# Performance work log

Measured on AMD Instinct MI355X. Metric: run time of the kernel, lower is better.

Reference implementation:

```python
import jax, jax.numpy as jnp
import numpy as np

E = 8        # num_experts
TOP_K = 2
DIM = 1024
DFF = DIM // 4
T = 32768    # batch*seq tokens


def setup_inputs() -> dict:
    key = jax.random.key(0)
    ks = jax.random.split(key, 5)
    x = jax.random.normal(ks[0], (T, DIM), dtype=jnp.float32)
    router_w = jax.random.normal(ks[1], (E, DIM), dtype=jnp.float32) * 0.02
    w1 = jax.random.normal(ks[2], (E, DIM, DFF), dtype=jnp.float32) * 0.02
    w2 = jax.random.normal(ks[3], (E, DFF, DIM), dtype=jnp.float32) * 0.02
    w3 = jax.random.normal(ks[4], (E, DIM, DFF), dtype=jnp.float32) * 0.02
    return {"x": x, "router_w": router_w, "w1": w1, "w2": w2, "w3": w3}


def reference(x, router_w, w1, w2, w3):
    # ---- Router ----
    logits = x @ router_w.T                          # [T, E]
    scores = jax.nn.softmax(logits.astype(jnp.float32), axis=1)
    # expert_bias is zero at init and noise_scale=0 -> topk on raw scores
    _, sel = jax.lax.top_k(scores, TOP_K)            # [T, K] expert indices
    top_scores = jnp.take_along_axis(scores, sel, axis=-1)
    top_scores = top_scores / jnp.sum(top_scores, axis=-1, keepdims=True)

    flat_experts = sel.reshape(-1)                   # [T*K]
    sorted_idx = jnp.argsort(flat_experts)           # stable sort, expert-centric order
    scatter_idx = sorted_idx // TOP_K                # original token id per row
    num_tokens_per_expert = jnp.bincount(flat_experts, length=E).astype(jnp.int32)

    x_gathered = x[scatter_idx]                      # [T*K, DIM]
    scores_sorted = top_scores.reshape(-1)[sorted_idx]  # [T*K]

    # ---- GroupedExpert: grouped GEMM SwiGLU in bf16 ----
    xb = x_gathered.astype(jnp.bfloat16)
    x1 = jax.lax.ragged_dot(xb, w1.astype(jnp.bfloat16), num_tokens_per_expert)
    x3 = jax.lax.ragged_dot(xb, w3.astype(jnp.bfloat16), num_tokens_per_expert)
    h = jax.nn.silu(x1) * x3                         # [T*K, DFF] bf16
    expert_out = jax.lax.ragged_dot(h, w2.astype(jnp.bfloat16), num_tokens_per_expert)
    expert_out = expert_out.astype(x.dtype)          # [T*K, DIM]

    # ---- Combine: weighted scatter-add back to token positions ----
    out = jnp.zeros_like(x).at[scatter_idx].add(expert_out * scores_sorted[:, None])
    return out
```

## Files before the change

### kernel.cpp

```cpp
#include <hip/hip_runtime.h>
#include <cstdint>
#include <cstddef>
#include <math.h>

#define T_TOK 32768
#define DIM   1024
#define DFF   256
#define NE    8
#define NB    16
#define ROWS  (T_TOK * 2)
#define MAXROWS 66560
#define MAXTILES (MAXROWS / 64)

typedef unsigned short u16;
typedef __attribute__((ext_vector_type(8))) short v8s;
typedef __attribute__((ext_vector_type(4))) float v4f;

__device__ __forceinline__ u16 f2bf(float f) {
  union { float f; unsigned u; } v; v.f = f;
  return (u16)((v.u + 0x7FFFu + ((v.u >> 16) & 1u)) >> 16);
}
__device__ __forceinline__ float bf2f(u16 b) {
  union { unsigned u; float f; } v; v.u = ((unsigned)b) << 16; return v.f;
}

__device__ __forceinline__ void gload16(const u16* g, u16* l) {
  __builtin_amdgcn_global_load_lds(
      (const __attribute__((address_space(1))) void*)g,
      (__attribute__((address_space(3))) void*)l, 16, 0, 0);
}

#define WS_W13  ((size_t)0)
#define WS_W2T  ((size_t)8388608)
#define WS_H    ((size_t)12582912)
#define WS_Y    ((size_t)46661632)
#define WS_RTOK ((size_t)182976512)
#define WS_POS  ((size_t)183242752)
#define WS_CNT  ((size_t)183504896)
#define WS_CUR  ((size_t)183504960)
#define WS_OFF  ((size_t)183505024)
#define WS_SEL  ((size_t)183505152)
#define WS_WTS  ((size_t)183767296)
#define WS_XB   WS_Y

__global__ __launch_bounds__(256) void k_pack13(const float* __restrict__ w1,
                                                const float* __restrict__ w3,
                                                u16* __restrict__ W13p) {
  __shared__ float s1[32][33];
  __shared__ float s3[32][33];
  int e = blockIdx.z, k0 = blockIdx.x * 32, j0w = blockIdx.y;
  int tx = threadIdx.x, ty = threadIdx.y;
  size_t wbase = (size_t)e * DIM * DFF;
#pragma unroll
  for (int r = 0; r < 4; ++r) {
    int kl = ty + 8 * r;
    size_t src = wbase + (size_t)(k0 + kl) * DFF + j0w * 32 + tx;
    s1[kl][tx] = w1[src];
    s3[kl][tx] = w3[src];
  }
  __syncthreads();
  size_t obase = (size_t)e * 512 * 1024;
#pragma unroll
  for (int r = 0; r < 4; ++r) {
    int jl = ty + 8 * r;
    int n1 = 64 * j0w + jl;
    W13p[obase + (size_t)n1 * 1024 + k0 + tx]        = f2bf(s1[tx][jl]);
    W13p[obase + (size_t)(n1 + 32) * 1024 + k0 + tx] = f2bf(s3[tx][jl]);
  }
}

__global__ __launch_bounds__(256) void k_pack2(const float* __restrict__ w2,
                                               u16* __restrict__ W2t) {
  __shared__ float s[32][33];
  int e = blockIdx.z, k0 = blockIdx.x * 32, n0 = blockIdx.y * 32;
  int tx = threadIdx.x, ty = threadIdx.y;
#pragma unroll
  for (int r = 0; r < 4; ++r) {
    int kl = ty + 8 * r;
    s[kl][tx] = w2[(size_t)e * DFF * DIM + (size_t)(k0 + kl) * DIM + n0 + tx];
  }
  __syncthreads();
#pragma unroll
  for (int r = 0; r < 4; ++r) {
    int nl = ty + 8 * r;
    W2t[(size_t)e * DIM * DFF + (size_t)(n0 + nl) * DFF + k0 + tx] = f2bf(s[tx][nl]);
  }
}

__global__ __launch_bounds__(256) void k_router(const float* __restrict__ x,
                                                const float* __restrict__ rw,
                                                int* __restrict__ sel,
                                                float* __restrict__ wts,
                                                int* __restrict__ cnt,
                                                u16* __restrict__ xb) {
  __shared__ __align__(16) float s_rw[NE][1028];
  __shared__ __align__(16) float s_x[32][132];
  __shared__ float s_lg[256];
  __shared__ int s_cnt[NB];
  int tid = threadIdx.x;
  if (tid < NB) s_cnt[tid] = 0;
  {
    const float4* rw4 = (const float4*)rw;
#pragma unroll
    for (int r = 0; r < 8; ++r)
      *(float4*)(&s_rw[r][tid * 4]) = rw4[r * 256 + tid];
  }
  int tl = tid >> 3, e = tid & 7;
  float acc = 0.0f;
  const float4* x4 = (const float4*)x;
  for (int c = 0; c < 8; ++c) {
    __syncthreads();
#pragma unroll
    for (int j = 0; j < 4; ++j) {
      int slot = j * 256 + tid;
      int t = slot >> 5, kk = (slot & 31) * 4;
      *(float4*)(&s_x[t][kk]) = x4[((size_t)blockIdx.x * 32 + t) * 256 + c * 32 + (slot & 31)];
    }
    __syncthreads();
    const float* xp = &s_x[tl][0];
    const float* wp = &s_rw[e][c * 128];
#pragma unroll 16
    for (int k = 0; k < 128; ++k) acc = fmaf(xp[k], wp[k], acc);
    {
      int t2 = tid >> 3, k2 = (tid & 7) * 16;
      const float* sp = &s_x[t2][k2];
      u16 tb[16];
#pragma unroll
      for (int k = 0; k < 16; ++k) tb[k] = f2bf(sp[k]);
      u16* xo = xb + ((size_t)(blockIdx.x * 32 + t2)) * 1024 + c * 128 + k2;
      *(uint4*)(xo)     = *(const uint4*)(&tb[0]);
      *(uint4*)(xo + 8) = *(const uint4*)(&tb[8]);
    }
  }
  s_lg[tid] = acc;
  __syncthreads();
  if ((tid & 7) == 0) {
    int t = blockIdx.x * 32 + tl;
    const float* lg = s_lg + tid;
    int b0 = 0; float v0 = lg[0];
#pragma unroll
    for (int ee = 1; ee < NE; ++ee) if (lg[ee] > v0) { v0 = lg[ee]; b0 = ee; }
    int b1 = -1; float v1 = -1e30f;
#pragma unroll
    for (int ee = 0; ee < NE; ++ee) if (ee != b0 && lg[ee] > v1) { v1 = lg[ee]; b1 = ee; }
    float w0 = 1.0f / (1.0f + expf(v1 - v0));
    sel[2 * t] = b0; sel[2 * t + 1] = b1;
    wts[2 * t] = w0; wts[2 * t + 1] = 1.0f - w0;
    atomicAdd(&s_cnt[2 * b0], 1);
    atomicAdd(&s_cnt[2 * b1 + 1], 1);
  }
  __syncthreads();
  if (tid < NB && s_cnt[tid]) atomicAdd(&cnt[tid], s_cnt[tid]);
}

__global__ void k_scan(const int* __restrict__ cnt, int* __restrict__ offs) {
  if (threadIdx.x == 0 && blockIdx.x == 0) {
    int o = 0;
#pragma unroll
    for (int b = 0; b < NB; ++b) { offs[b] = o; o += (cnt[b] + 63) & ~63; }
    offs[NB] = o;
  }
}

__global__ __launch_bounds__(256) void k_scatter(const int* __restrict__ sel,
                                                 const int* __restrict__ offs,
                                                 int* __restrict__ cursor,
                                                 int* __restrict__ rtok,
                                                 int* __restrict__ pos) {
  __shared__ int s_cnt[NB], s_base[NB];
  int tid = threadIdx.x;
  if (tid < NB) s_cnt[tid] = 0;
  __syncthreads();
  int g = blockIdx.x * 256 + tid;
  int b = sel[g] * 2 + (g & 1);
  int lpos = atomicAdd(&s_cnt[b], 1);
  __syncthreads();
  if (tid < NB) s_base[tid] = s_cnt[tid] ? atomicAdd(&cursor[tid], s_cnt[tid]) : 0;
  __syncthreads();
  int row = offs[b] + s_base[b] + lpos;
  rtok[row] = g >> 1;
  pos[g] = row;
}

__global__ __launch_bounds__(512, 4) void k_gemm1(const u16* __restrict__ xb,
                                                  const u16* __restrict__ W13p,
                                                  const int* __restrict__ rtok,
                                                  const int* __restrict__ offs,
                                                  u16* __restrict__ h) {
  __shared__ __align__(16) u16 A_s[64][32];
  __shared__ __align__(16) u16 B_s[512][32];
  int bx = (int)((blockIdx.x & 7) * (MAXTILES / 8) + (blockIdx.x >> 3));
  int row0 = bx * 64;
  if (row0 >= offs[NB]) return;
  int b2 = 0;
  while (row0 >= offs[b2 + 1]) ++b2;
  int e = b2 >> 1;
  int tid = threadIdx.x;
  int wv = tid >> 6, lane = tid & 63;
  int lr = lane & 15, q = lane >> 4;
  int qa = q ^ ((lr >> 1) & 3);
  int srow = lane >> 2;
  int schk = (lane & 3) ^ ((lane >> 3) & 3);
  const u16* srcB = W13p + (size_t)e * 512 * 1024
                  + (size_t)(64 * wv + srow) * 1024 + schk * 8;
  int arow = (wv >= 4) ? (16 * (wv - 4) + srow) : srow;
  int tk = rtok[row0 + arow]; if (tk < 0) tk = 0;
  const u16* srcA = xb + (size_t)tk * 1024 + schk * 8;
  u16* ldsB = &B_s[64 * wv][0];
  u16* ldsA = &A_s[(wv & 3) * 16][0];
  v4f acc[4][4] = {};
  for (int k0 = 0; k0 < DIM; k0 += 32) {
#pragma unroll
    for (int i = 0; i < 4; ++i)
      gload16(srcB + (size_t)i * 16 * 1024 + k0, ldsB + i * 512);
    if (wv >= 4) gload16(srcA + k0, ldsA);
    __syncthreads();
    v8s a[4], b[4];
#pragma unroll
    for (int mt = 0; mt < 4; ++mt) a[mt] = *(const v8s*)(&A_s[16 * mt + lr][qa * 8]);
#pragma unroll
    for (int nt = 0; nt < 4; ++nt) b[nt] = *(const v8s*)(&B_s[64 * wv + 16 * nt + lr][qa * 8]);
#pragma unroll
    for (int mt = 0; mt < 4; ++mt)
#pragma unroll
      for (int nt = 0; nt < 4; ++nt)
        acc[mt][nt] = __builtin_amdgcn_mfma_f32_16x16x32_bf16(a[mt], b[nt], acc[mt][nt], 0, 0, 0);
    __syncthreads();
  }
#pragma unroll
  for (int mt = 0; mt < 4; ++mt)
#pragma unroll
    for (int nt = 0; nt < 2; ++nt)
#pragma unroll
      for (int r = 0; r < 4; ++r) {
        float x1 = bf2f(f2bf(acc[mt][nt][r]));
        float x3 = bf2f(f2bf(acc[mt][nt + 2][r]));
        float hv = x1 * x3 / (1.0f + __expf(-x1));
        int row = row0 + 16 * mt + q * 4 + r;
        int col = 32 * wv + 16 * nt + lr;
        h[(size_t)row * DFF + col] = f2bf(hv);
      }
}

__global__ __launch_bounds__(512, 4) void k_gemm2(const u16* __restrict__ h,
                                                  const u16* __restrict__ W2t,
                                                  const int* __restrict__ offs,
                                                  u16* __restrict__ y) {
  __shared__ __align__(16) u16 A_s[64][32];
  __shared__ __align__(16) u16 B_s[512][32];
  int bx = (int)((blockIdx.x & 7) * (MAXTILES / 8) + (blockIdx.x >> 3));
  int row0 = bx * 64;
  if (row0 >= offs[NB]) return;
  int b2 = 0;
  while (row0 >= offs[b2 + 1]) ++b2;
  int e = b2 >> 1;
  int nb = blockIdx.y;
  int tid = threadIdx.x;
  int wv = tid >> 6, lane = tid & 63;
  int lr = lane & 15, q = lane >> 4;
  int qa = q ^ ((lr >> 1) & 3);
  int srow = lane >> 2;
  int schk = (lane & 3) ^ ((lane >> 3) & 3);
  const u16* srcB = W2t + (size_t)e * DIM * DFF + (size_t)nb * 512 * DFF
                  + (size_t)(64 * wv + srow) * DFF + schk * 8;
  int arow = (wv >= 4) ? (16 * (wv - 4) + srow) : srow;
  const u16* srcA = h + (size_t)(row0 + arow) * DFF + schk * 8;
  u16* ldsB = &B_s[64 * wv][0];
  u16* ldsA = &A_s[(wv & 3) * 16][0];
  v4f acc[4][4] = {};
  for (int k0 = 0; k0 < DFF; k0 += 32) {
#pragma unroll
    for (int i = 0; i < 4; ++i)
      gload16(srcB + (size_t)i * 16 * DFF + k0, ldsB + i * 512);
    if (wv >= 4) gload16(srcA + k0, ldsA);
    __syncthreads();
    v8s a[4], b[4];
#pragma unroll
    for (int mt = 0; mt < 4; ++mt) a[mt] = *(const v8s*)(&A_s[16 * mt + lr][qa * 8]);
#pragma unroll
    for (int nt = 0; nt < 4; ++nt) b[nt] = *(const v8s*)(&B_s[64 * wv + 16 * nt + lr][qa * 8]);
#pragma unroll
    for (int mt = 0; mt < 4; ++mt)
#pragma unroll
      for (int nt = 0; nt < 4; ++nt)
        acc[mt][nt] = __builtin_amdgcn_mfma_f32_16x16x32_bf16(a[mt], b[nt], acc[mt][nt], 0, 0, 0);
    __syncthreads();
  }
  u16* Ts = &B_s[0][0];
#pragma unroll
  for (int mt = 0; mt < 4; ++mt) {
#pragma unroll
    for (int nt = 0; nt < 4; ++nt)
#pragma unroll
      for (int r = 0; r < 4; ++r)
        Ts[(q * 4 + r) * 520 + 64 * wv + 16 * nt + lr] = f2bf(acc[mt][nt][r]);
    __syncthreads();
#pragma unroll
    for (int i = 0; i < 2; ++i) {
      int j = tid + 512 * i;
      int rr = j >> 6, cc = j & 63;
      uint4 v = *(const uint4*)(Ts + rr * 520 + cc * 8);
      *(uint4*)(y + (size_t)(row0 + 16 * mt + rr) * 1024 + nb * 512 + cc * 8) = v;
    }
    __syncthreads();
  }
}

__global__ __launch_bounds__(256) void k_combine(const u16* __restrict__ y,
                                                 const int* __restrict__ pos,
                                                 const float* __restrict__ wts,
                                                 float* __restrict__ out) {
  int tid = threadIdx.x, wv = tid >> 6, lane = tid & 63;
  int t = blockIdx.x * 4 + wv;
  int r0 = pos[2 * t], r1 = pos[2 * t + 1];
  float w0 = wts[2 * t], w1 = wts[2 * t + 1];
  const uint4* y0 = (const uint4*)(y + (size_t)r0 * 1024);
  const uint4* y1 = (const uint4*)(y + (size_t)r1 * 1024);
  float* o = out + (size_t)t * 1024;
#pragma unroll
  for (int i = 0; i < 2; ++i) {
    int j = lane + 64 * i;
    uint4 a = y0[j], b = y1[j];
    const u16* pa = (const u16*)&a;
    const u16* pb = (const u16*)&b;
    float f[8];
#pragma unroll
    for (int k = 0; k < 8; ++k) f[k] = bf2f(pa[k]) * w0 + bf2f(pb[k]) * w1;
    *(float4*)(o + j * 8)     = *(float4*)&f[0];
    *(float4*)(o + j * 8 + 4) = *(float4*)&f[4];
  }
}

extern "C" void kernel_launch(void* const* d_in, const int* in_sizes, int n_in,
                              void* d_out, int out_size, void* d_ws, size_t ws_size,
                              hipStream_t stream) {
  (void)in_sizes; (void)n_in; (void)ws_size; (void)out_size;
  const float* x  = (const float*)d_in[0];
  const float* rw = (const float*)d_in[1];
  const float* w1 = (const float*)d_in[2];
  const float* w2 = (const float*)d_in[3];
  const float* w3 = (const float*)d_in[4];
  float* out = (float*)d_out;
  char* ws = (char*)d_ws;
  u16*   W13p = (u16*)(ws + WS_W13);
  u16*   W2t  = (u16*)(ws + WS_W2T);
  u16*   hbuf = (u16*)(ws + WS_H);
  u16*   ybuf = (u16*)(ws + WS_Y);
  u16*   xbuf = (u16*)(ws + WS_XB);
  int*   rtok = (int*)(ws + WS_RTOK);
  int*   pos  = (int*)(ws + WS_POS);
  int*   cnt  = (int*)(ws + WS_CNT);
  int*   cur  = (int*)(ws + WS_CUR);
  int*   offs = (int*)(ws + WS_OFF);
  int*   sel  = (int*)(ws + WS_SEL);
  float* wts  = (float*)(ws + WS_WTS);

  hipMemsetAsync(ws + WS_RTOK, 0xFF, (size_t)MAXROWS * 4, stream);
  hipMemsetAsync(ws + WS_CNT, 0, 128, stream);

  k_pack13<<<dim3(32, 8, 8), dim3(32, 8), 0, stream>>>(w1, w3, W13p);
  k_pack2 <<<dim3(8, 32, 8), dim3(32, 8), 0, stream>>>(w2, W2t);
  k_router<<<dim3(T_TOK / 32), dim3(256), 0, stream>>>(x, rw, sel, wts, cnt, xbuf);
  k_scan  <<<dim3(1), dim3(64), 0, stream>>>(cnt, offs);
  k_scatter<<<dim3(ROWS / 256), dim3(256), 0, stream>>>(sel, offs, cur, rtok, pos);
  k_gemm1 <<<dim3(MAXTILES), dim3(512), 0, stream>>>(xbuf, W13p, rtok, offs, hbuf);
  k_gemm2 <<<dim3(MAXTILES, 2), dim3(512), 0, stream>>>(hbuf, W2t, offs, ybuf);
  k_combine<<<dim3(T_TOK / 4), dim3(256), 0, stream>>>(ybuf, pos, wts, out);
}
```

Before: 494.1 us.

## Double-buffer LDS tiles in both grouped GEMM kernels to overlap loads with MFMA

Both grouped GEMM kernels now keep two LDS buffers for the A and B tiles. Each iteration issues the global-to-LDS loads for the next K slice before running the MFMAs on the current one, and replaces the two __syncthreads per iteration with one waitcnt plus barrier. The goal is to hide global load latency behind matrix compute. In exchange it doubles LDS use per block, which may lower occupancy under launch_bounds(512,4), and it relies on hand-placed waitcnt and sched_barrier for correctness.

```diff
diff --git a/kernel.cpp b/kernel.cpp
--- a/kernel.cpp
+++ b/kernel.cpp
@@ -187,8 +187,8 @@
                                                   const int* __restrict__ rtok,
                                                   const int* __restrict__ offs,
                                                   u16* __restrict__ h) {
-  __shared__ __align__(16) u16 A_s[64][32];
-  __shared__ __align__(16) u16 B_s[512][32];
+  __shared__ __align__(16) u16 A_s[2][64][32];
+  __shared__ __align__(16) u16 B_s[2][512][32];
   int bx = (int)((blockIdx.x & 7) * (MAXTILES / 8) + (blockIdx.x >> 3));
   int row0 = bx * 64;
   if (row0 >= offs[NB]) return;
@@ -206,27 +206,47 @@
   int arow = (wv >= 4) ? (16 * (wv - 4) + srow) : srow;
   int tk = rtok[row0 + arow]; if (tk < 0) tk = 0;
   const u16* srcA = xb + (size_t)tk * 1024 + schk * 8;
-  u16* ldsB = &B_s[64 * wv][0];
-  u16* ldsA = &A_s[(wv & 3) * 16][0];
   v4f acc[4][4] = {};
-  for (int k0 = 0; k0 < DIM; k0 += 32) {
-#pragma unroll
-    for (int i = 0; i < 4; ++i)
-      gload16(srcB + (size_t)i * 16 * 1024 + k0, ldsB + i * 512);
-    if (wv >= 4) gload16(srcA + k0, ldsA);
-    __syncthreads();
-    v8s a[4], b[4];
-#pragma unroll
-    for (int mt = 0; mt < 4; ++mt) a[mt] = *(const v8s*)(&A_s[16 * mt + lr][qa * 8]);
-#pragma unroll
-    for (int nt = 0; nt < 4; ++nt) b[nt] = *(const v8s*)(&B_s[64 * wv + 16 * nt + lr][qa * 8]);
-#pragma unroll
-    for (int mt = 0; mt < 4; ++mt)
-#pragma unroll
-      for (int nt = 0; nt < 4; ++nt)
-        acc[mt][nt] = __builtin_amdgcn_mfma_f32_16x16x32_bf16(a[mt], b[nt], acc[mt][nt], 0, 0, 0);
-    __syncthreads();
-  }
+
+#define G1_STAGE(buf, k0) do {                                              \
+    u16* ldsB_ = &B_s[buf][64 * wv][0];                                     \
+    _Pragma("unroll")                                                       \
+    for (int i_ = 0; i_ < 4; ++i_)                                          \
+      gload16(srcB + (size_t)i_ * 16 * 1024 + (k0), ldsB_ + i_ * 512);      \
+    if (wv >= 4) gload16(srcA + (k0), &A_s[buf][(wv & 3) * 16][0]);         \
+  } while (0)
+
+#define G1_COMP(buf) do {                                                   \
+    v8s a_[4], b_[4];                                                       \
+    _Pragma("unroll")                                                       \
+    for (int mt_ = 0; mt_ < 4; ++mt_)                                       \
+      a_[mt_] = *(const v8s*)(&A_s[buf][16 * mt_ + lr][qa * 8]);            \
+    _Pragma("unroll")                                                       \
+    for (int nt_ = 0; nt_ < 4; ++nt_)                                       \
+      b_[nt_] = *(const v8s*)(&B_s[buf][64 * wv + 16 * nt_ + lr][qa * 8]);  \
+    _Pragma("unroll")                                                       \
+    for (int mt_ = 0; mt_ < 4; ++mt_)                                       \
+      _Pragma("unroll")                                                     \
+      for (int nt_ = 0; nt_ < 4; ++nt_)                                     \
+        acc[mt_][nt_] = __builtin_amdgcn_mfma_f32_16x16x32_bf16(            \
+            a_[mt_], b_[nt_], acc[mt_][nt_], 0, 0, 0);                      \
+  } while (0)
+
+  G1_STAGE(0, 0);
+  asm volatile("s_waitcnt vmcnt(0)" ::: "memory");
+  __builtin_amdgcn_s_barrier();
+  __builtin_amdgcn_sched_barrier(0);
+#pragma unroll 2
+  for (int t = 0; t < 31; ++t) {
+    int cur = t & 1;
+    G1_STAGE(cur ^ 1, (t + 1) * 32);
+    G1_COMP(cur);
+    asm volatile("s_waitcnt vmcnt(0)" ::: "memory");
+    __builtin_amdgcn_s_barrier();
+    __builtin_amdgcn_sched_barrier(0);
+  }
+  G1_COMP(1);
+
 #pragma unroll
   for (int mt = 0; mt < 4; ++mt)
 #pragma unroll
@@ -240,14 +260,16 @@
         int col = 32 * wv + 16 * nt + lr;
         h[(size_t)row * DFF + col] = f2bf(hv);
       }
+#undef G1_STAGE
+#undef G1_COMP
 }
 
 __global__ __launch_bounds__(512, 4) void k_gemm2(const u16* __restrict__ h,
                                                   const u16* __restrict__ W2t,
                                                   const int* __restrict__ offs,
                                                   u16* __restrict__ y) {
-  __shared__ __align__(16) u16 A_s[64][32];
-  __shared__ __align__(16) u16 B_s[512][32];
+  __shared__ __align__(16) u16 A_s[2][64][32];
+  __shared__ __align__(16) u16 B_s[2][512][32];
   int bx = (int)((blockIdx.x & 7) * (MAXTILES / 8) + (blockIdx.x >> 3));
   int row0 = bx * 64;
   if (row0 >= offs[NB]) return;
@@ -265,28 +287,49 @@
                   + (size_t)(64 * wv + srow) * DFF + schk * 8;
   int arow = (wv >= 4) ? (16 * (wv - 4) + srow) : srow;
   const u16* srcA = h + (size_t)(row0 + arow) * DFF + schk * 8;
-  u16* ldsB = &B_s[64 * wv][0];
-  u16* ldsA = &A_s[(wv & 3) * 16][0];
   v4f acc[4][4] = {};
-  for (int k0 = 0; k0 < DFF; k0 += 32) {
-#pragma unroll
-    for (int i = 0; i < 4; ++i)
-      gload16(srcB + (size_t)i * 16 * DFF + k0, ldsB + i * 512);
-    if (wv >= 4) gload16(srcA + k0, ldsA);
-    __syncthreads();
-    v8s a[4], b[4];
-#pragma unroll
-    for (int mt = 0; mt < 4; ++mt) a[mt] = *(const v8s*)(&A_s[16 * mt + lr][qa * 8]);
-#pragma unroll
-    for (int nt = 0; nt < 4; ++nt) b[nt] = *(const v8s*)(&B_s[64 * wv + 16 * nt + lr][qa * 8]);
-#pragma unroll
-    for (int mt = 0; mt < 4; ++mt)
-#pragma unroll
-      for (int nt = 0; nt < 4; ++nt)
-        acc[mt][nt] = __builtin_amdgcn_mfma_f32_16x16x32_bf16(a[mt], b[nt], acc[mt][nt], 0, 0, 0);
-    __syncthreads();
-  }
-  u16* Ts = &B_s[0][0];
+
+#define G2_STAGE(buf, k0) do {                                              \
+    u16* ldsB_ = &B_s[buf][64 * wv][0];                                     \
+    _Pragma("unroll")                                                       \
+    for (int i_ = 0; i_ < 4; ++i_)                                          \
+      gload16(srcB + (size_t)i_ * 16 * DFF + (k0), ldsB_ + i_ * 512);       \
+    if (wv >= 4) gload16(srcA + (k0), &A_s[buf][(wv & 3) * 16][0]);         \
+  } while (0)
+
+#define G2_COMP(buf) do {                                                   \
+    v8s a_[4], b_[4];                                                       \
+    _Pragma("unroll")                                                       \
+    for (int mt_ = 0; mt_ < 4; ++mt_)                                       \
+      a_[mt_] = *(const v8s*)(&A_s[buf][16 * mt_ + lr][qa * 8]);            \
+    _Pragma("unroll")                                                       \
+    for (int nt_ = 0; nt_ < 4; ++nt_)                                       \
+      b_[nt_] = *(const v8s*)(&B_s[buf][64 * wv + 16 * nt_ + lr][qa * 8]);  \
+    _Pragma("unroll")                                                       \
+    for (int mt_ = 0; mt_ < 4; ++mt_)                                       \
+      _Pragma("unroll")                                                     \
+      for (int nt_ = 0; nt_ < 4; ++nt_)                                     \
+        acc[mt_][nt_] = __builtin_amdgcn_mfma_f32_16x16x32_bf16(            \
+            a_[mt_], b_[nt_], acc[mt_][nt_], 0, 0, 0);                      \
+  } while (0)
+
+  G2_STAGE(0, 0);
+  asm volatile("s_waitcnt vmcnt(0)" ::: "memory");
+  __builtin_amdgcn_s_barrier();
+  __builtin_amdgcn_sched_barrier(0);
+#pragma unroll 2
+  for (int t = 0; t < 7; ++t) {
+    int cur = t & 1;
+    G2_STAGE(cur ^ 1, (t + 1) * 32);
+    G2_COMP(cur);
+    asm volatile("s_waitcnt vmcnt(0)" ::: "memory");
+    __builtin_amdgcn_s_barrier();
+    __builtin_amdgcn_sched_barrier(0);
+  }
+  G2_COMP(1);
+  __syncthreads();
+
+  u16* Ts = &B_s[0][0][0];
 #pragma unroll
   for (int mt = 0; mt < 4; ++mt) {
 #pragma unroll
@@ -304,6 +347,8 @@
     }
     __syncthreads();
   }
+#undef G2_STAGE
+#undef G2_COMP
 }
 
 __global__ __launch_bounds__(256) void k_combine(const u16* __restrict__ y,
```

Result: no change. 489.2 us (-1.0%).
